# Performance work log

Hardware: AMD Instinct MI355X
Metric: run time of the kernel (lower is better)

## Reference

```python
import jax, jax.numpy as jnp
import numpy as np

BS, NQ, DIMS = 4, 6400, 256
NH, NL, NP, NQUEUE = 8, 1, 4, 2


def ms_deform_attn(value, shapes_np, starts_np, loc, attn):
    # value: [B, Nv, H, D]; loc: [B, Nq, H, L, P, 2] in [0,1]; attn: [B, Nq, H, L, P]
    B, Nv, H, D = value.shape
    _, Nq, _, L, P, _ = loc.shape
    out = jnp.zeros((B, H, Nq, D), loc.dtype)
    for l in range(L):
        Hl, Wl = int(shapes_np[l, 0]), int(shapes_np[l, 1])
        s = int(starts_np[l])
        vl = value[:, s:s + Hl * Wl].transpose(0, 2, 1, 3)  # [B,H,HW,D]
        # grid_sample align_corners=False pixel coords
        x = loc[:, :, :, l, :, 0] * Wl - 0.5  # [B,Nq,H,P]
        y = loc[:, :, :, l, :, 1] * Hl - 0.5
        x0 = jnp.floor(x); y0 = jnp.floor(y)
        dx = x - x0; dy = y - y0
        x0i = x0.astype(jnp.int32); y0i = y0.astype(jnp.int32)
        acc = jnp.zeros((B, H, Nq * P, D), loc.dtype)
        corners = [(x0i, y0i, (1 - dx) * (1 - dy)),
                   (x0i + 1, y0i, dx * (1 - dy)),
                   (x0i, y0i + 1, (1 - dx) * dy),
                   (x0i + 1, y0i + 1, dx * dy)]
        for xi, yi, w in corners:
            valid = (xi >= 0) & (xi < Wl) & (yi >= 0) & (yi < Hl)
            idx = jnp.clip(yi, 0, Hl - 1) * Wl + jnp.clip(xi, 0, Wl - 1)  # [B,Nq,H,P]
            idx_t = idx.transpose(0, 2, 1, 3).reshape(B, H, Nq * P, 1)
            g = jnp.take_along_axis(vl, idx_t, axis=2)  # [B,H,Nq*P,D]
            wv = jnp.where(valid, w, 0.0).transpose(0, 2, 1, 3).reshape(B, H, Nq * P, 1)
            acc = acc + g * wv
        acc = acc.reshape(B, H, Nq, P, D)
        wl = attn[:, :, :, l].transpose(0, 2, 1, 3)  # [B,H,Nq,P]
        out = out + jnp.einsum('bhnpd,bhnp->bhnd', acc, wl)
    return out.transpose(0, 2, 1, 3).reshape(B, Nq, H * D)


def setup_inputs() -> dict:
    key = jax.random.key(0)
    ks = jax.random.split(key, 12)
    d2 = DIMS * NQUEUE
    noff = NQUEUE * NH * NL * NP * 2
    nattn = NQUEUE * NH * NL * NP
    sc = 1.0 / np.sqrt(DIMS)
    return {
        'query': jax.random.normal(ks[0], (BS, NQ, DIMS), jnp.float32),
        'voxbev': jax.random.normal(ks[1], (BS, NQ, DIMS), jnp.float32),
        'reference_points': jax.random.uniform(ks[2], (BS * NQUEUE, NQ, NL, 2), jnp.float32),
        'spatial_shapes': jnp.array([[80, 80]], dtype=jnp.int64),
        'level_start_index': jnp.array([0], dtype=jnp.int64),
        'Wv': jax.random.normal(ks[3], (DIMS, DIMS), jnp.float32) * sc,
        'bv': jax.random.normal(ks[4], (DIMS,), jnp.float32) * 0.01,
        'Woff': jax.random.normal(ks[5], (d2, noff), jnp.float32) * (1.0 / np.sqrt(d2)),
        'boff': jax.random.normal(ks[6], (noff,), jnp.float32),
        'Wattn': jax.random.normal(ks[7], (d2, nattn), jnp.float32) * (1.0 / np.sqrt(d2)),
        'battn': jax.random.normal(ks[8], (nattn,), jnp.float32) * 0.01,
        'Wo': jax.random.normal(ks[9], (DIMS, DIMS), jnp.float32) * sc,
        'bo': jax.random.normal(ks[10], (DIMS,), jnp.float32) * 0.01,
    }


def reference(query, voxbev, reference_points, spatial_shapes, level_start_index,
              Wv, bv, Woff, boff, Wattn, battn, Wo, bo):
    bs, nq, dims = query.shape
    shapes_np = np.asarray(spatial_shapes)
    starts_np = np.asarray(level_start_index)
    identity = query
    # value = stack([query, voxbev], 1).reshape(bs*2, nq, dims) -> interleaved [q0,v0,q1,v1,...]
    value = jnp.stack([query, voxbev], 1).reshape(bs * NQUEUE, nq, dims)
    qcat = jnp.concatenate([value[:bs], query], -1)  # [bs, nq, 2*dims]
    v = (value @ Wv + bv).reshape(bs * NQUEUE, nq, NH, dims // NH)
    off = (qcat @ Woff + boff).reshape(bs, nq, NH, NQUEUE, NL, NP, 2)
    attn = (qcat @ Wattn + battn).reshape(bs, nq, NH, NQUEUE, NL * NP)
    attn = jax.nn.softmax(attn, axis=-1).reshape(bs, nq, NH, NQUEUE, NL, NP)
    attn = attn.transpose(0, 3, 1, 2, 4, 5).reshape(bs * NQUEUE, nq, NH, NL, NP)
    off = off.transpose(0, 3, 1, 2, 4, 5, 6).reshape(bs * NQUEUE, nq, NH, NL, NP, 2)
    # offset normalizer: (W, H) per level
    norm = jnp.stack([spatial_shapes[:, 1], spatial_shapes[:, 0]], -1).astype(off.dtype)  # [L,2]
    loc = reference_points[:, :, None, :, None, :] + off / norm[None, None, None, :, None, :]
    out = ms_deform_attn(v, shapes_np, starts_np, loc, attn)  # [bs*2, nq, dims]
    out = out.reshape(bs, NQUEUE, nq, dims).mean(1)  # mean over queue
    out = out @ Wo + bo
    return out + identity  # dropout is identity in eval
```

## Files before the change

kernel.cpp:

```cpp
#include <hip/hip_runtime.h>
#include <hip/hip_bf16.h>

#define BS   4
#define NQ   6400
#define DIMS 256
#define NH   8
#define NP   4
#define GW   80
#define GH   80

typedef __hip_bfloat16 bf16;
typedef unsigned short ushort;
typedef __attribute__((ext_vector_type(8))) short short8;
typedef __attribute__((ext_vector_type(4))) float floatx4;

union bfu { bf16 h; ushort s; };
__device__ __forceinline__ ushort f2bs(float x) { bfu u; u.h = __float2bfloat16(x); return u.s; }
__device__ __forceinline__ float bs2f(ushort s) { return __uint_as_float(((unsigned)s) << 16); }
__device__ __forceinline__ float ldin(const void* p, size_t i, int isf) {
    return isf ? ((const float*)p)[i] : bs2f(((const ushort*)p)[i]);
}

__device__ __forceinline__ void gl_lds16(const void* gsrc, void* ldst) {
    __builtin_amdgcn_global_load_lds(
        (const __attribute__((address_space(1))) unsigned int*)gsrc,
        (__attribute__((address_space(3))) unsigned int*)ldst,
        16, 0, 0);
}

__device__ __forceinline__ int self_detect(const ushort* __restrict__ q, int tid) {
    int bad = 0;
    const uint4 u0 = ((const uint4*)q)[tid * 2];
    const uint4 u1 = ((const uint4*)q)[tid * 2 + 1];
    const unsigned w[8] = { u0.x, u0.y, u0.z, u0.w, u1.x, u1.y, u1.z, u1.w };
    #pragma unroll
    for (int j = 0; j < 8; ++j) {
        if (((w[j] >> 7)  & 0xFF) > 160) bad = 1;
        if (((w[j] >> 23) & 0xFF) > 160) bad = 1;
    }
    return __any(bad) ? 1 : 0;
}

__global__ __launch_bounds__(256) void prep_k(
    const void* __restrict__ Wv, const void* __restrict__ bv,
    const void* __restrict__ Woff, const void* __restrict__ boff,
    const void* __restrict__ Wattn, const void* __restrict__ battn,
    const void* __restrict__ Wo, const void* __restrict__ bo,
    int* __restrict__ flagp,
    ushort* __restrict__ WvT, ushort* __restrict__ WoaT, ushort* __restrict__ WoT,
    float* __restrict__ biasv, float* __restrict__ biasoa, float* __restrict__ biaso,
    const void* __restrict__ query, const void* __restrict__ voxbev,
    uint4* __restrict__ qb, uint4* __restrict__ vbv)
{
    const int tid = threadIdx.x;
    const int isf = self_detect((const ushort*)query, tid);
    const int bid = blockIdx.x;
    if (bid == 0 && tid == 0) *flagp = isf;
    if (bid < 899) {
        const int i = bid * 256 + tid;
        const int n1 = 256 * 256, n2 = n1 + 192 * 512, n3 = n2 + 256 * 256;
        const int n4 = n3 + 256, n5 = n4 + 192, n6 = n5 + 256;
        if (i < n1) {
            int n = i >> 8, k = i & 255;
            WvT[i] = f2bs(ldin(Wv, (size_t)k * 256 + n, isf));
        } else if (i < n2) {
            int j = i - n1, n = j >> 9, k = j & 511;
            float v = (n < 128) ? ldin(Woff, (size_t)k * 128 + n, isf)
                                : ldin(Wattn, (size_t)k * 64 + (n - 128), isf);
            WoaT[j] = f2bs(v);
        } else if (i < n3) {
            int j = i - n2, n = j >> 8, k = j & 255;
            WoT[j] = f2bs(ldin(Wo, (size_t)k * 256 + n, isf));
        } else if (i < n4) {
            biasv[i - n3] = ldin(bv, i - n3, isf);
        } else if (i < n5) {
            int j = i - n4;
            biasoa[j] = (j < 128) ? ldin(boff, j, isf) : ldin(battn, j - 128, isf);
        } else if (i < n6) {
            biaso[i - n5] = ldin(bo, i - n5, isf);
        }
    } else {
        if (isf == 0) return;
        const int t = (bid - 899) * 256 + tid;
        const int half = 819200;
        const void* src = (t < half) ? query : voxbev;
        uint4* dst = (t < half) ? qb : vbv;
        const int j = (t < half) ? t : t - half;
        const float4* s = (const float4*)src + (size_t)j * 2;
        float4 a = s[0], b = s[1];
        uint4 o;
        o.x = ((unsigned)f2bs(a.y) << 16) | f2bs(a.x);
        o.y = ((unsigned)f2bs(a.w) << 16) | f2bs(a.z);
        o.z = ((unsigned)f2bs(b.y) << 16) | f2bs(b.x);
        o.w = ((unsigned)f2bs(b.w) << 16) | f2bs(b.z);
        dst[j] = o;
    }
}

enum { A_VAL = 0, A_QCAT = 1, A_PLAIN = 2 };
enum { O_BF16 = 0, O_FINAL = 1, O_VPERM = 2, O_OAPERM = 3 };

#define BKS  128
#define ABYT (128 * 256)
#define SMEMB (ABYT + 2 * 64 * 256)

template <int AMODE, int OMODE, int KTOT, int NW, int NXW, int MG>
__device__ __forceinline__ void pgemm_body(
    const int F, char* smem,
    const ushort* __restrict__ Apl, const ushort* __restrict__ BT,
    const float* __restrict__ biasf, void* __restrict__ C,
    const void* __restrict__ query_raw, const void* __restrict__ voxbev_raw,
    const ushort* __restrict__ qb, const ushort* __restrict__ vbv,
    const int isf)
{
    constexpr int N = NW * 64 * NXW;
    constexpr int TW = NW * 64;
    constexpr int NT = KTOT / BKS;
    constexpr int CSTW = (NW == 1) ? 67 : 131;
    char* abuf = smem;
    char* bbuf = smem + ABYT;
    float* cbf = (float*)smem;

    const int xcd = F & 7, l = F >> 3;
    const int n = l % NXW;
    const int mg = (l / NXW) * 8 + xcd;
    if (mg >= MG) return;
    const int bm = mg * 128, bn = n * TW;

    const int tid = threadIdx.x;
    const int lane = tid & 63, wv = tid >> 6;
    const int wm = wv * 32;
    const int fr = lane & 15;
    const int srow = lane >> 4;
    const int sslot = lane & 15;

    const ushort* qsrc = isf ? qb  : (const ushort*)query_raw;
    const ushort* vsrc = isf ? vbv : (const ushort*)voxbev_raw;
    const ushort* aph[2] = { nullptr, nullptr };
    if (AMODE == A_PLAIN) {
        aph[0] = Apl + (size_t)bm * DIMS;
    } else {
        const int b = bm / NQ, q0 = bm - (bm / NQ) * NQ;
        aph[0] = ((b & 1) ? vsrc : qsrc) + (size_t)((b >> 1) * NQ + q0) * DIMS;
        if (AMODE == A_QCAT) aph[1] = qsrc + (size_t)(b * NQ + q0) * DIMS;
    }

    floatx4 acc[2][4 * NW] = {};

    #pragma unroll
    for (int t = 0; t < NT; ++t) {
        if (t > 0) __syncthreads();
        #pragma unroll
        for (int c8 = 0; c8 < 8; ++c8) {
            const int c = wv * 8 + c8;
            const int row = c * 4 + srow;
            const int g = sslot ^ (row & 15);
            const int k = t * BKS + g * 8;
            const ushort* gp;
            if (AMODE == A_QCAT && KTOT == 512)
                gp = aph[k >> 8] + (size_t)row * DIMS + (k & 255);
            else
                gp = aph[0] + (size_t)row * DIMS + k;
            gl_lds16(gp, abuf + c * 1024);
        }
        #pragma unroll
        for (int cb = 0; cb < 4 * NW; ++cb) {
            const int c = wv * 4 * NW + cb;
            const int row = c * 4 + srow;
            const int g = sslot ^ (row & 15);
            gl_lds16(&BT[(size_t)(bn + row) * KTOT + t * BKS + g * 8],
                     bbuf + c * 1024);
        }
        asm volatile("s_waitcnt vmcnt(0)" ::: "memory");
        __syncthreads();

        #pragma unroll
        for (int k0 = 0; k0 < BKS; k0 += 32) {
            const int gl = (k0 >> 3) + (lane >> 4);
            const int sl = gl ^ fr;
            short8 af[2], bf[4 * NW];
            #pragma unroll
            for (int mt = 0; mt < 2; ++mt)
                af[mt] = *(const short8*)(abuf + (wm + mt * 16 + fr) * 256
                                               + sl * 16);
            #pragma unroll
            for (int nt = 0; nt < 4 * NW; ++nt)
                bf[nt] = *(const short8*)(bbuf + (nt * 16 + fr) * 256
                                               + sl * 16);
            #pragma unroll
            for (int mt = 0; mt < 2; ++mt)
                #pragma unroll
                for (int nt = 0; nt < 4 * NW; ++nt)
                    acc[mt][nt] = __builtin_amdgcn_mfma_f32_16x16x32_bf16(
                        af[mt], bf[nt], acc[mt][nt], 0, 0, 0);
        }
    }

    const int col = lane & 15, rq = (lane >> 4) * 4;

    if (NW == 1) {
        __syncthreads();
        #pragma unroll
        for (int mt = 0; mt < 2; ++mt)
            #pragma unroll
            for (int nt = 0; nt < 4; ++nt)
                #pragma unroll
                for (int r = 0; r < 4; ++r)
                    cbf[(wm + mt * 16 + rq + r) * 67 + nt * 16 + col] =
                        acc[mt][nt][r];
        __syncthreads();

        if (OMODE == O_FINAL && isf) {
            const int r16 = tid >> 4, cc = tid & 15;
            #pragma unroll
            for (int it = 0; it < 8; ++it) {
                const int lr = it * 16 + r16;
                const size_t g = (size_t)(bm + lr);
                float4 x = *(const float4*)&cbf[lr * 67 + cc * 4];
                const ushort* rs = qsrc + g * DIMS + bn + cc * 4;
                x.x += biasf[bn + cc * 4 + 0] + bs2f(rs[0]);
                x.y += biasf[bn + cc * 4 + 1] + bs2f(rs[1]);
                x.z += biasf[bn + cc * 4 + 2] + bs2f(rs[2]);
                x.w += biasf[bn + cc * 4 + 3] + bs2f(rs[3]);
                *(float4*)((float*)C + g * N + bn + cc * 4) = x;
            }
        } else {
            const int r8 = tid >> 3, c8 = tid & 7;
            #pragma unroll
            for (int it = 0; it < 4; ++it) {
                const int lr = it * 32 + r8;
                const size_t g = (size_t)(bm + lr);
                float4 x0 = *(const float4*)&cbf[lr * 67 + c8 * 8];
                float4 x1 = *(const float4*)&cbf[lr * 67 + c8 * 8 + 4];
                float xs[8] = { x0.x, x0.y, x0.z, x0.w, x1.x, x1.y, x1.z, x1.w };
                #pragma unroll
                for (int e = 0; e < 8; ++e) xs[e] += biasf[bn + c8 * 8 + e];
                if (OMODE == O_FINAL) {
                    const ushort* rs = qsrc + g * DIMS + bn + c8 * 8;
                    #pragma unroll
                    for (int e = 0; e < 8; ++e) xs[e] += bs2f(rs[e]);
                }
                uint4 o;
                o.x = ((unsigned)f2bs(xs[1]) << 16) | f2bs(xs[0]);
                o.y = ((unsigned)f2bs(xs[3]) << 16) | f2bs(xs[2]);
                o.z = ((unsigned)f2bs(xs[5]) << 16) | f2bs(xs[4]);
                o.w = ((unsigned)f2bs(xs[7]) << 16) | f2bs(xs[6]);
                ushort* dstp;
                if (OMODE == O_VPERM) {
                    const int cc = bn + c8 * 8;
                    const int s = (int)(g / NQ), qq = (int)(g % NQ);
                    dstp = (ushort*)C + ((size_t)(s * 8 + (cc >> 5)) * NQ + qq) * 32
                                      + (cc & 31);
                } else if (OMODE == O_OAPERM) {
                    const int cc = bn + c8 * 8;
                    const int bb = (int)(g / NQ), qq = (int)(g % NQ);
                    int hh, off;
                    if (cc < 128) { hh = cc >> 4; off = cc & 15; }
                    else          { hh = (cc - 128) >> 3; off = 16; }
                    dstp = (ushort*)C + ((size_t)(bb * 8 + hh) * NQ + qq) * 24 + off;
                } else {
                    dstp = (ushort*)C + g * N + bn + c8 * 8;
                }
                *(uint4*)dstp = o;
            }
        }
    } else {
        const int lbase = wm & 63;
        #pragma unroll
        for (int half = 0; half < 2; ++half) {
            __syncthreads();
            if ((wv >> 1) == half) {
                #pragma unroll
                for (int mt = 0; mt < 2; ++mt)
                    #pragma unroll
                    for (int nt = 0; nt < 8; ++nt)
                        #pragma unroll
                        for (int r = 0; r < 4; ++r)
                            cbf[(lbase + mt * 16 + rq + r) * 131 + nt * 16 + col] =
                                acc[mt][nt][r];
            }
            __syncthreads();

            if (OMODE == O_FINAL && isf) {
                const int r32 = tid >> 5, cc = tid & 31;
                #pragma unroll
                for (int it = 0; it < 8; ++it) {
                    const int lr = it * 8 + r32;
                    const size_t g = (size_t)(bm + half * 64 + lr);
                    float4 x = *(const float4*)&cbf[lr * 131 + cc * 4];
                    const ushort* rs = qsrc + g * DIMS + bn + cc * 4;
                    x.x += biasf[bn + cc * 4 + 0] + bs2f(rs[0]);
                    x.y += biasf[bn + cc * 4 + 1] + bs2f(rs[1]);
                    x.z += biasf[bn + cc * 4 + 2] + bs2f(rs[2]);
                    x.w += biasf[bn + cc * 4 + 3] + bs2f(rs[3]);
                    *(float4*)((float*)C + g * N + bn + cc * 4) = x;
                }
            } else {
                const int r16 = tid >> 4, cc = tid & 15;
                #pragma unroll
                for (int it = 0; it < 4; ++it) {
                    const int lr = it * 16 + r16;
                    const size_t g = (size_t)(bm + half * 64 + lr);
                    float4 x0 = *(const float4*)&cbf[lr * 131 + cc * 8];
                    float4 x1 = *(const float4*)&cbf[lr * 131 + cc * 8 + 4];
                    float xs[8] = { x0.x, x0.y, x0.z, x0.w, x1.x, x1.y, x1.z, x1.w };
                    #pragma unroll
                    for (int e = 0; e < 8; ++e) xs[e] += biasf[bn + cc * 8 + e];
                    if (OMODE == O_FINAL) {
                        const ushort* rs = qsrc + g * DIMS + bn + cc * 8;
                        #pragma unroll
                        for (int e = 0; e < 8; ++e) xs[e] += bs2f(rs[e]);
                    }
                    uint4 o;
                    o.x = ((unsigned)f2bs(xs[1]) << 16) | f2bs(xs[0]);
                    o.y = ((unsigned)f2bs(xs[3]) << 16) | f2bs(xs[2]);
                    o.z = ((unsigned)f2bs(xs[5]) << 16) | f2bs(xs[4]);
                    o.w = ((unsigned)f2bs(xs[7]) << 16) | f2bs(xs[6]);
                    ushort* dstp;
                    if (OMODE == O_VPERM) {
                        const int cc2 = bn + cc * 8;
                        const int s = (int)(g / NQ), qq = (int)(g % NQ);
                        dstp = (ushort*)C
                             + ((size_t)(s * 8 + (cc2 >> 5)) * NQ + qq) * 32
                             + (cc2 & 31);
                    } else {
                        dstp = (ushort*)C + g * N + bn + cc * 8;
                    }
                    *(uint4*)dstp = o;
                }
            }
        }
    }
}

__global__ __launch_bounds__(256) void gemm12_k(
    const ushort* __restrict__ WvT, const float* __restrict__ biasv,
    ushort* __restrict__ v_ws,
    const ushort* __restrict__ WoaT, const float* __restrict__ biasoa,
    ushort* __restrict__ offraw,
    const void* __restrict__ query_raw, const void* __restrict__ voxbev_raw,
    const ushort* __restrict__ qb, const ushort* __restrict__ vbv,
    const int* __restrict__ flagp)
{
    __shared__ __align__(16) char smem[SMEMB];
    const int isf = *flagp;
    const int bid = blockIdx.x;
    if (bid < 800) {
        pgemm_body<A_VAL, O_VPERM, 256, 2, 2, 400>(bid, smem,
            nullptr, WvT, biasv, (void*)v_ws, query_raw, voxbev_raw, qb, vbv, isf);
    } else {
        pgemm_body<A_QCAT, O_OAPERM, 512, 1, 3, 200>(bid - 800, smem,
            nullptr, WoaT, biasoa, (void*)offraw, query_raw, voxbev_raw, qb, vbv, isf);
    }
}

__global__ __launch_bounds__(256) void gemm4_k(
    const ushort* __restrict__ Apl, const ushort* __restrict__ BT,
    const float* __restrict__ biasf, void* __restrict__ C,
    const void* __restrict__ query_raw, const void* __restrict__ voxbev_raw,
    const ushort* __restrict__ qb, const ushort* __restrict__ vbv,
    const int* __restrict__ flagp)
{
    __shared__ __align__(16) char smem[SMEMB];
    const int isf = *flagp;
    pgemm_body<A_PLAIN, O_FINAL, 256, 2, 2, 200>(blockIdx.x, smem,
        Apl, BT, biasf, C, query_raw, voxbev_raw, qb, vbv, isf);
}

__global__ __launch_bounds__(256) void sample_k(
    const ushort* __restrict__ v,
    const ushort* __restrict__ offp,
    const void* __restrict__ refpts,
    const int* __restrict__ flagp,
    ushort* __restrict__ sampled)
{
    const int isf = *flagp;
    __shared__ int   sidx[64][2][17];
    __shared__ float swt [64][2][17];
    const int tid = threadIdx.x;
    const int j = blockIdx.x;
    const int h = j & 7;
    const int k = j >> 3;
    const int b = k / 100;
    const int q0 = (k % 100) * 64;

    if (tid < 128) {
        const int lq = tid >> 1, queue = tid & 1;
        const int q = q0 + lq;
        const ushort* rec = offp + ((size_t)(b * 8 + h) * NQ + q) * 24;
        const ushort* al = rec + 16 + queue * 4;
        float l0 = bs2f(al[0]), l1 = bs2f(al[1]), l2 = bs2f(al[2]), l3 = bs2f(al[3]);
        float mx = fmaxf(fmaxf(l0, l1), fmaxf(l2, l3));
        float e0 = __expf(l0 - mx), e1 = __expf(l1 - mx);
        float e2 = __expf(l2 - mx), e3 = __expf(l3 - mx);
        float inv = 0.5f / (e0 + e1 + e2 + e3);
        const int bq = b * 2 + queue;
        const float rx = ldin(refpts, ((size_t)bq * NQ + q) * 2 + 0, isf);
        const float ry = ldin(refpts, ((size_t)bq * NQ + q) * 2 + 1, isf);
        const ushort* od = rec + queue * 8;
        float ww[4] = { e0 * inv, e1 * inv, e2 * inv, e3 * inv };
        #pragma unroll
        for (int p = 0; p < NP; ++p) {
            const float x = rx * (float)GW + bs2f(od[p * 2 + 0]) - 0.5f;
            const float y = ry * (float)GH + bs2f(od[p * 2 + 1]) - 0.5f;
            const float x0f = floorf(x), y0f = floorf(y);
            const float dx = x - x0f, dy = y - y0f;
            const int x0 = (int)x0f, y0 = (int)y0f;
            const float wp = ww[p];
            const float cw4[4] = { wp * (1.0f - dx) * (1.0f - dy),
                                   wp * dx * (1.0f - dy),
                                   wp * (1.0f - dx) * dy,
                                   wp * dx * dy };
            #pragma unroll
            for (int c = 0; c < 4; ++c) {
                const int xs = x0 + (c & 1), ys = y0 + (c >> 1);
                const bool ok = (unsigned)xs < (unsigned)GW && (unsigned)ys < (unsigned)GH;
                const int xi = min(max(xs, 0), GW - 1);
                const int yi = min(max(ys, 0), GH - 1);
                sidx[lq][queue][p * 4 + c] = yi * GW + xi;
                swt [lq][queue][p * 4 + c] = ok ? cw4[c] : 0.0f;
            }
        }
    }
    __syncthreads();

    const int lq = tid >> 2, d8 = tid & 3;
    const int q = q0 + lq;
    float a[8] = {};
    #pragma unroll
    for (int queue = 0; queue < 2; ++queue) {
        const ushort* vb = v + (((size_t)(b * 2 + queue) * 8 + h) * NQ) * 32 + d8 * 8;
        #pragma unroll
        for (int hf = 0; hf < 2; ++hf) {
            uint4 g[8];
            #pragma unroll
            for (int u = 0; u < 8; ++u) {
                const int ci = sidx[lq][queue][hf * 8 + u];
                g[u] = *(const uint4*)&vb[(size_t)ci * 32];
            }
            __builtin_amdgcn_sched_barrier(0);
            #pragma unroll
            for (int u = 0; u < 8; ++u) {
                const float cw = swt[lq][queue][hf * 8 + u];
                a[0] += cw * bs2f((ushort)g[u].x); a[1] += cw * bs2f((ushort)(g[u].x >> 16));
                a[2] += cw * bs2f((ushort)g[u].y); a[3] += cw * bs2f((ushort)(g[u].y >> 16));
                a[4] += cw * bs2f((ushort)g[u].z); a[5] += cw * bs2f((ushort)(g[u].z >> 16));
                a[6] += cw * bs2f((ushort)g[u].w); a[7] += cw * bs2f((ushort)(g[u].w >> 16));
            }
        }
    }
    uint4 o;
    o.x = ((unsigned)f2bs(a[1]) << 16) | f2bs(a[0]);
    o.y = ((unsigned)f2bs(a[3]) << 16) | f2bs(a[2]);
    o.z = ((unsigned)f2bs(a[5]) << 16) | f2bs(a[4]);
    o.w = ((unsigned)f2bs(a[7]) << 16) | f2bs(a[6]);
    *(uint4*)&sampled[((size_t)b * NQ + q) * DIMS + h * 32 + d8 * 8] = o;
}

extern "C" void kernel_launch(void* const* d_in, const int* in_sizes, int n_in,
                              void* d_out, int out_size, void* d_ws, size_t ws_size,
                              hipStream_t stream)
{
    const void* query  = d_in[0];
    const void* voxbev = d_in[1];
    const void* refpts = d_in[2];
    const void* Wv   = d_in[5];  const void* bv    = d_in[6];
    const void* Woff = d_in[7];  const void* boff  = d_in[8];
    const void* Wattn= d_in[9];  const void* battn = d_in[10];
    const void* Wo   = d_in[11]; const void* bo    = d_in[12];

    char* p = (char*)d_ws;
    int* flag = (int*)p;             p += 256;
    ushort* WvT  = (ushort*)p;       p += 256 * 256 * 2;
    ushort* WoaT = (ushort*)p;       p += 192 * 512 * 2;
    ushort* WoT  = (ushort*)p;       p += 256 * 256 * 2;
    float* biasv  = (float*)p;       p += 1024;
    float* biasoa = (float*)p;       p += 1024;
    float* biaso  = (float*)p;       p += 1024;
    ushort* qb   = (ushort*)p;       p += (size_t)BS * NQ * DIMS * 2;
    ushort* vbv  = (ushort*)p;       p += (size_t)BS * NQ * DIMS * 2;
    ushort* v_ws = (ushort*)p;       p += (size_t)2 * BS * NQ * DIMS * 2;
    ushort* offraw = (ushort*)p;     p += (size_t)BS * NQ * 192 * 2;
    ushort* sampled = (ushort*)p;

    prep_k<<<7299, 256, 0, stream>>>(Wv, bv, Woff, boff, Wattn, battn, Wo, bo,
                                     flag, WvT, WoaT, WoT, biasv, biasoa, biaso,
                                     query, voxbev, (uint4*)qb, (uint4*)vbv);

    gemm12_k<<<1400, 256, 0, stream>>>(WvT, biasv, v_ws, WoaT, biasoa, offraw,
                                       query, voxbev, qb, vbv, flag);

    sample_k<<<3200, 256, 0, stream>>>(v_ws, offraw, refpts, flag, sampled);

    gemm4_k<<<400, 256, 0, stream>>>(sampled, WoT, biaso, d_out,
                                     query, voxbev, qb, vbv, flag);
}
```

Before: 181.9 us.

## Double-buffer gemm12 K-loop with 64-wide tiles and async LDS prefetch

Replaces the single-buffered 128-K-step GEMM in gemm12 with a double-buffered pipeline using 64-wide K steps and 128x64 output tiles. The next stage's global-to-LDS loads are issued before computing the current one, using partial vmcnt waits, so load latency overlaps MFMA work. LDS use drops to 48KB and the V-projection grid grows from 800 to 1600 blocks, which may raise occupancy. The final GEMM keeps the old wide path via a separate specialized template. Costs are more barriers per K element and smaller tiles that reload A more often.

```diff
diff --git a/kernel.cpp b/kernel.cpp
--- a/kernel.cpp
+++ b/kernel.cpp
@@ -26,6 +26,12 @@
         (const __attribute__((address_space(1))) unsigned int*)gsrc,
         (__attribute__((address_space(3))) unsigned int*)ldst,
         16, 0, 0);
+}
+
+__device__ __forceinline__ void barrier_fence() {
+    __builtin_amdgcn_sched_barrier(0);
+    asm volatile("s_barrier" ::: "memory");
+    __builtin_amdgcn_sched_barrier(0);
 }
 
 __device__ __forceinline__ int self_detect(const ushort* __restrict__ q, int tid) {
@@ -100,12 +106,11 @@
 enum { A_VAL = 0, A_QCAT = 1, A_PLAIN = 2 };
 enum { O_BF16 = 0, O_FINAL = 1, O_VPERM = 2, O_OAPERM = 3 };
 
-#define BKS  128
-#define ABYT (128 * 256)
-#define SMEMB (ABYT + 2 * 64 * 256)
-
-template <int AMODE, int OMODE, int KTOT, int NW, int NXW, int MG>
-__device__ __forceinline__ void pgemm_body(
+#define PTILE 24576
+#define PSMEM (2 * PTILE)
+
+template <int AMODE, int OMODE, int KTOT, int NXW, int MG>
+__device__ __forceinline__ void pgemm_pipe(
     const int F, char* smem,
     const ushort* __restrict__ Apl, const ushort* __restrict__ BT,
     const float* __restrict__ biasf, void* __restrict__ C,
@@ -113,26 +118,23 @@
     const ushort* __restrict__ qb, const ushort* __restrict__ vbv,
     const int isf)
 {
-    constexpr int N = NW * 64 * NXW;
-    constexpr int TW = NW * 64;
-    constexpr int NT = KTOT / BKS;
-    constexpr int CSTW = (NW == 1) ? 67 : 131;
-    char* abuf = smem;
-    char* bbuf = smem + ABYT;
+    constexpr int N = 64 * NXW;
+    constexpr int NT = KTOT / 64;
     float* cbf = (float*)smem;
 
     const int xcd = F & 7, l = F >> 3;
     const int n = l % NXW;
     const int mg = (l / NXW) * 8 + xcd;
     if (mg >= MG) return;
-    const int bm = mg * 128, bn = n * TW;
+    const int bm = mg * 128, bn = n * 64;
 
     const int tid = threadIdx.x;
     const int lane = tid & 63, wv = tid >> 6;
     const int wm = wv * 32;
     const int fr = lane & 15;
-    const int srow = lane >> 4;
-    const int sslot = lane & 15;
+    const int lrow = lane >> 3;
+    const int lslot = lane & 7;
+    const int sg = lslot ^ lrow;
 
     const ushort* qsrc = isf ? qb  : (const ushort*)query_raw;
     const ushort* vsrc = isf ? vbv : (const ushort*)voxbev_raw;
@@ -145,7 +147,180 @@
         if (AMODE == A_QCAT) aph[1] = qsrc + (size_t)(b * NQ + q0) * DIMS;
     }
 
-    floatx4 acc[2][4 * NW] = {};
+    auto stage = [&](int td, int t) {
+        char* ab = smem + td * PTILE;
+        char* bb = ab + 16384;
+        #pragma unroll
+        for (int c4 = 0; c4 < 4; ++c4) {
+            const int c = wv * 4 + c4;
+            const int row = c * 8 + lrow;
+            const int k = t * 64 + sg * 8;
+            const ushort* gp;
+            if (AMODE == A_QCAT && KTOT == 512)
+                gp = aph[k >> 8] + (size_t)row * DIMS + (k & 255);
+            else
+                gp = aph[0] + (size_t)row * DIMS + k;
+            gl_lds16(gp, ab + c * 1024);
+        }
+        #pragma unroll
+        for (int c2 = 0; c2 < 2; ++c2) {
+            const int c = wv * 2 + c2;
+            const int row = c * 8 + lrow;
+            gl_lds16(&BT[(size_t)(bn + row) * KTOT + t * 64 + sg * 8],
+                     bb + c * 1024);
+        }
+    };
+
+    floatx4 acc[2][4] = {};
+
+    stage(0, 0);
+    #pragma unroll
+    for (int t = 0; t < NT; ++t) {
+        if (t + 1 < NT) {
+            stage((t + 1) & 1, t + 1);
+            __builtin_amdgcn_sched_barrier(0);
+            asm volatile("s_waitcnt vmcnt(6)" ::: "memory");
+        } else {
+            __builtin_amdgcn_sched_barrier(0);
+            asm volatile("s_waitcnt vmcnt(0)" ::: "memory");
+        }
+        barrier_fence();
+
+        const short* acur = (const short*)(smem + (t & 1) * PTILE);
+        const short* bcur = acur + 8192;
+        #pragma unroll
+        for (int k0 = 0; k0 < 64; k0 += 32) {
+            const int gl = (k0 >> 3) + (lane >> 4);
+            const int sl = gl ^ (fr & 7);
+            short8 af[2], bf[4];
+            #pragma unroll
+            for (int mt = 0; mt < 2; ++mt)
+                af[mt] = *(const short8*)&acur[(wm + mt * 16 + fr) * 64 + sl * 8];
+            #pragma unroll
+            for (int nt = 0; nt < 4; ++nt)
+                bf[nt] = *(const short8*)&bcur[(nt * 16 + fr) * 64 + sl * 8];
+            #pragma unroll
+            for (int mt = 0; mt < 2; ++mt)
+                #pragma unroll
+                for (int nt = 0; nt < 4; ++nt)
+                    acc[mt][nt] = __builtin_amdgcn_mfma_f32_16x16x32_bf16(
+                        af[mt], bf[nt], acc[mt][nt], 0, 0, 0);
+        }
+        barrier_fence();
+    }
+
+    __syncthreads();
+    const int col = lane & 15, rq = (lane >> 4) * 4;
+    #pragma unroll
+    for (int mt = 0; mt < 2; ++mt)
+        #pragma unroll
+        for (int nt = 0; nt < 4; ++nt)
+            #pragma unroll
+            for (int r = 0; r < 4; ++r)
+                cbf[(wm + mt * 16 + rq + r) * 67 + nt * 16 + col] = acc[mt][nt][r];
+    __syncthreads();
+
+    if (OMODE == O_FINAL && isf) {
+        const int r16 = tid >> 4, cc = tid & 15;
+        #pragma unroll
+        for (int it = 0; it < 8; ++it) {
+            const int lr = it * 16 + r16;
+            const size_t g = (size_t)(bm + lr);
+            float4 x = *(const float4*)&cbf[lr * 67 + cc * 4];
+            const ushort* rs = qsrc + g * DIMS + bn + cc * 4;
+            x.x += biasf[bn + cc * 4 + 0] + bs2f(rs[0]);
+            x.y += biasf[bn + cc * 4 + 1] + bs2f(rs[1]);
+            x.z += biasf[bn + cc * 4 + 2] + bs2f(rs[2]);
+            x.w += biasf[bn + cc * 4 + 3] + bs2f(rs[3]);
+            *(float4*)((float*)C + g * N + bn + cc * 4) = x;
+        }
+    } else {
+        const int r8 = tid >> 3, c8 = tid & 7;
+        #pragma unroll
+        for (int it = 0; it < 4; ++it) {
+            const int lr = it * 32 + r8;
+            const size_t g = (size_t)(bm + lr);
+            float4 x0 = *(const float4*)&cbf[lr * 67 + c8 * 8];
+            float4 x1 = *(const float4*)&cbf[lr * 67 + c8 * 8 + 4];
+            float xs[8] = { x0.x, x0.y, x0.z, x0.w, x1.x, x1.y, x1.z, x1.w };
+            #pragma unroll
+            for (int e = 0; e < 8; ++e) xs[e] += biasf[bn + c8 * 8 + e];
+            if (OMODE == O_FINAL) {
+                const ushort* rs = qsrc + g * DIMS + bn + c8 * 8;
+                #pragma unroll
+                for (int e = 0; e < 8; ++e) xs[e] += bs2f(rs[e]);
+            }
+            uint4 o;
+            o.x = ((unsigned)f2bs(xs[1]) << 16) | f2bs(xs[0]);
+            o.y = ((unsigned)f2bs(xs[3]) << 16) | f2bs(xs[2]);
+            o.z = ((unsigned)f2bs(xs[5]) << 16) | f2bs(xs[4]);
+            o.w = ((unsigned)f2bs(xs[7]) << 16) | f2bs(xs[6]);
+            ushort* dstp;
+            if (OMODE == O_VPERM) {
+                const int cc = bn + c8 * 8;
+                const int s = (int)(g / NQ), qq = (int)(g % NQ);
+                dstp = (ushort*)C + ((size_t)(s * 8 + (cc >> 5)) * NQ + qq) * 32
+                                  + (cc & 31);
+            } else if (OMODE == O_OAPERM) {
+                const int cc = bn + c8 * 8;
+                const int bb = (int)(g / NQ), qq = (int)(g % NQ);
+                int hh, off;
+                if (cc < 128) { hh = cc >> 4; off = cc & 15; }
+                else          { hh = (cc - 128) >> 3; off = 16; }
+                dstp = (ushort*)C + ((size_t)(bb * 8 + hh) * NQ + qq) * 24 + off;
+            } else {
+                dstp = (ushort*)C + g * N + bn + c8 * 8;
+            }
+            *(uint4*)dstp = o;
+        }
+    }
+}
+
+#define BKS  128
+#define ABYT (128 * 256)
+#define WSMEM (ABYT + 2 * 64 * 256)
+
+template <int AMODE, int OMODE, int KTOT, int MG>
+__device__ __forceinline__ void pgemm_wide(
+    const int F, char* smem,
+    const ushort* __restrict__ Apl, const ushort* __restrict__ BT,
+    const float* __restrict__ biasf, void* __restrict__ C,
+    const void* __restrict__ query_raw, const void* __restrict__ voxbev_raw,
+    const ushort* __restrict__ qb, const ushort* __restrict__ vbv,
+    const int isf)
+{
+    constexpr int NXW = 2;
+    constexpr int N = 256;
+    constexpr int NT = KTOT / BKS;
+    char* abuf = smem;
+    char* bbuf = smem + ABYT;
+    float* cbf = (float*)smem;
+
+    const int xcd = F & 7, l = F >> 3;
+    const int n = l % NXW;
+    const int mg = (l / NXW) * 8 + xcd;
+    if (mg >= MG) return;
+    const int bm = mg * 128, bn = n * 128;
+
+    const int tid = threadIdx.x;
+    const int lane = tid & 63, wv = tid >> 6;
+    const int wm = wv * 32;
+    const int fr = lane & 15;
+    const int srow = lane >> 4;
+    const int sslot = lane & 15;
+
+    const ushort* qsrc = isf ? qb  : (const ushort*)query_raw;
+    const ushort* vsrc = isf ? vbv : (const ushort*)voxbev_raw;
+    const ushort* aph[2] = { nullptr, nullptr };
+    if (AMODE == A_PLAIN) {
+        aph[0] = Apl + (size_t)bm * DIMS;
+    } else {
+        const int b = bm / NQ, q0 = bm - (bm / NQ) * NQ;
+        aph[0] = ((b & 1) ? vsrc : qsrc) + (size_t)((b >> 1) * NQ + q0) * DIMS;
+        if (AMODE == A_QCAT) aph[1] = qsrc + (size_t)(b * NQ + q0) * DIMS;
+    }
+
+    floatx4 acc[2][8] = {};
 
     #pragma unroll
     for (int t = 0; t < NT; ++t) {
@@ -156,16 +331,12 @@
             const int row = c * 4 + srow;
             const int g = sslot ^ (row & 15);
             const int k = t * BKS + g * 8;
-            const ushort* gp;
-            if (AMODE == A_QCAT && KTOT == 512)
-                gp = aph[k >> 8] + (size_t)row * DIMS + (k & 255);
-            else
-                gp = aph[0] + (size_t)row * DIMS + k;
+            const ushort* gp = aph[0] + (size_t)row * DIMS + k;
             gl_lds16(gp, abuf + c * 1024);
         }
         #pragma unroll
-        for (int cb = 0; cb < 4 * NW; ++cb) {
-            const int c = wv * 4 * NW + cb;
+        for (int cb = 0; cb < 8; ++cb) {
+            const int c = wv * 8 + cb;
             const int row = c * 4 + srow;
             const int g = sslot ^ (row & 15);
             gl_lds16(&BT[(size_t)(bn + row) * KTOT + t * BKS + g * 8],
@@ -178,45 +349,46 @@
         for (int k0 = 0; k0 < BKS; k0 += 32) {
             const int gl = (k0 >> 3) + (lane >> 4);
             const int sl = gl ^ fr;
-            short8 af[2], bf[4 * NW];
+            short8 af[2], bf[8];
             #pragma unroll
             for (int mt = 0; mt < 2; ++mt)
-                af[mt] = *(const short8*)(abuf + (wm + mt * 16 + fr) * 256
-                                               + sl * 16);
-            #pragma unroll
-            for (int nt = 0; nt < 4 * NW; ++nt)
-                bf[nt] = *(const short8*)(bbuf + (nt * 16 + fr) * 256
-                                               + sl * 16);
+                af[mt] = *(const short8*)(abuf + (wm + mt * 16 + fr) * 256 + sl * 16);
+            #pragma unroll
+            for (int nt = 0; nt < 8; ++nt)
+                bf[nt] = *(const short8*)(bbuf + (nt * 16 + fr) * 256 + sl * 16);
             #pragma unroll
             for (int mt = 0; mt < 2; ++mt)
                 #pragma unroll
-                for (int nt = 0; nt < 4 * NW; ++nt)
+                for (int nt = 0; nt < 8; ++nt)
                     acc[mt][nt] = __builtin_amdgcn_mfma_f32_16x16x32_bf16(
                         af[mt], bf[nt], acc[mt][nt], 0, 0, 0);
         }
     }
 
     const int col = lane & 15, rq = (lane >> 4) * 4;
-
-    if (NW == 1) {
+    const int lbase = wm & 63;
+    #pragma unroll
+    for (int half = 0; half < 2; ++half) {
         __syncthreads();
-        #pragma unroll
-        for (int mt = 0; mt < 2; ++mt)
-            #pragma unroll
-            for (int nt = 0; nt < 4; ++nt)
+        if ((wv >> 1) == half) {
+            #pragma unroll
+            for (int mt = 0; mt < 2; ++mt)
                 #pragma unroll
-                for (int r = 0; r < 4; ++r)
-                    cbf[(wm + mt * 16 + rq + r) * 67 + nt * 16 + col] =
-                        acc[mt][nt][r];
+                for (int nt = 0; nt < 8; ++nt)
+                    #pragma unroll
+                    for (int r = 0; r < 4; ++r)
+                        cbf[(lbase + mt * 16 + rq + r) * 131 + nt * 16 + col] =
+                            acc[mt][nt][r];
+        }
         __syncthreads();
 
         if (OMODE == O_FINAL && isf) {
-            const int r16 = tid >> 4, cc = tid & 15;
+            const int r32 = tid >> 5, cc = tid & 31;
             #pragma unroll
             for (int it = 0; it < 8; ++it) {
-                const int lr = it * 16 + r16;
-                const size_t g = (size_t)(bm + lr);
-                float4 x = *(const float4*)&cbf[lr * 67 + cc * 4];
+                const int lr = it * 8 + r32;
+                const size_t g = (size_t)(bm + half * 64 + lr);
+                float4 x = *(const float4*)&cbf[lr * 131 + cc * 4];
                 const ushort* rs = qsrc + g * DIMS + bn + cc * 4;
                 x.x += biasf[bn + cc * 4 + 0] + bs2f(rs[0]);
                 x.y += biasf[bn + cc * 4 + 1] + bs2f(rs[1]);
@@ -225,18 +397,18 @@
                 *(float4*)((float*)C + g * N + bn + cc * 4) = x;
             }
         } else {
-            const int r8 = tid >> 3, c8 = tid & 7;
+            const int r16 = tid >> 4, cc = tid & 15;
             #pragma unroll
             for (int it = 0; it < 4; ++it) {
-                const int lr = it * 32 + r8;
-                const size_t g = (size_t)(bm + lr);
-                float4 x0 = *(const float4*)&cbf[lr * 67 + c8 * 8];
-                float4 x1 = *(const float4*)&cbf[lr * 67 + c8 * 8 + 4];
+                const int lr = it * 16 + r16;
+                const size_t g = (size_t)(bm + half * 64 + lr);
+                float4 x0 = *(const float4*)&cbf[lr * 131 + cc * 8];
+                float4 x1 = *(const float4*)&cbf[lr * 131 + cc * 8 + 4];
                 float xs[8] = { x0.x, x0.y, x0.z, x0.w, x1.x, x1.y, x1.z, x1.w };
                 #pragma unroll
-                for (int e = 0; e < 8; ++e) xs[e] += biasf[bn + c8 * 8 + e];
+                for (int e = 0; e < 8; ++e) xs[e] += biasf[bn + cc * 8 + e];
                 if (OMODE == O_FINAL) {
-                    const ushort* rs = qsrc + g * DIMS + bn + c8 * 8;
+                    const ushort* rs = qsrc + g * DIMS + bn + cc * 8;
                     #pragma unroll
                     for (int e = 0; e < 8; ++e) xs[e] += bs2f(rs[e]);
                 }
@@ -247,87 +419,15 @@
                 o.w = ((unsigned)f2bs(xs[7]) << 16) | f2bs(xs[6]);
                 ushort* dstp;
                 if (OMODE == O_VPERM) {
-                    const int cc = bn + c8 * 8;
+                    const int cc2 = bn + cc * 8;
                     const int s = (int)(g / NQ), qq = (int)(g % NQ);
-                    dstp = (ushort*)C + ((size_t)(s * 8 + (cc >> 5)) * NQ + qq) * 32
-                                      + (cc & 31);
-                } else if (OMODE == O_OAPERM) {
-                    const int cc = bn + c8 * 8;
-                    const int bb = (int)(g / NQ), qq = (int)(g % NQ);
-                    int hh, off;
-                    if (cc < 128) { hh = cc >> 4; off = cc & 15; }
-                    else          { hh = (cc - 128) >> 3; off = 16; }
-                    dstp = (ushort*)C + ((size_t)(bb * 8 + hh) * NQ + qq) * 24 + off;
+                    dstp = (ushort*)C
+                         + ((size_t)(s * 8 + (cc2 >> 5)) * NQ + qq) * 32
+                         + (cc2 & 31);
                 } else {
-                    dstp = (ushort*)C + g * N + bn + c8 * 8;
+                    dstp = (ushort*)C + g * N + bn + cc * 8;
                 }
                 *(uint4*)dstp = o;
-            }
-        }
-    } else {
-        const int lbase = wm & 63;
-        #pragma unroll
-        for (int half = 0; half < 2; ++half) {
-            __syncthreads();
-            if ((wv >> 1) == half) {
-                #pragma unroll
-                for (int mt = 0; mt < 2; ++mt)
-                    #pragma unroll
-                    for (int nt = 0; nt < 8; ++nt)
-                        #pragma unroll
-                        for (int r = 0; r < 4; ++r)
-                            cbf[(lbase + mt * 16 + rq + r) * 131 + nt * 16 + col] =
-                                acc[mt][nt][r];
-            }
-            __syncthreads();
-
-            if (OMODE == O_FINAL && isf) {
-                const int r32 = tid >> 5, cc = tid & 31;
-                #pragma unroll
-                for (int it = 0; it < 8; ++it) {
-                    const int lr = it * 8 + r32;
-                    const size_t g = (size_t)(bm + half * 64 + lr);
-                    float4 x = *(const float4*)&cbf[lr * 131 + cc * 4];
-                    const ushort* rs = qsrc + g * DIMS + bn + cc * 4;
-                    x.x += biasf[bn + cc * 4 + 0] + bs2f(rs[0]);
-                    x.y += biasf[bn + cc * 4 + 1] + bs2f(rs[1]);
-                    x.z += biasf[bn + cc * 4 + 2] + bs2f(rs[2]);
-                    x.w += biasf[bn + cc * 4 + 3] + bs2f(rs[3]);
-                    *(float4*)((float*)C + g * N + bn + cc * 4) = x;
-                }
-            } else {
-                const int r16 = tid >> 4, cc = tid & 15;
-                #pragma unroll
-                for (int it = 0; it < 4; ++it) {
-                    const int lr = it * 16 + r16;
-                    const size_t g = (size_t)(bm + half * 64 + lr);
-                    float4 x0 = *(const float4*)&cbf[lr * 131 + cc * 8];
-                    float4 x1 = *(const float4*)&cbf[lr * 131 + cc * 8 + 4];
-                    float xs[8] = { x0.x, x0.y, x0.z, x0.w, x1.x, x1.y, x1.z, x1.w };
-                    #pragma unroll
-                    for (int e = 0; e < 8; ++e) xs[e] += biasf[bn + cc * 8 + e];
-                    if (OMODE == O_FINAL) {
-                        const ushort* rs = qsrc + g * DIMS + bn + cc * 8;
-                        #pragma unroll
-                        for (int e = 0; e < 8; ++e) xs[e] += bs2f(rs[e]);
-                    }
-                    uint4 o;
-                    o.x = ((unsigned)f2bs(xs[1]) << 16) | f2bs(xs[0]);
-                    o.y = ((unsigned)f2bs(xs[3]) << 16) | f2bs(xs[2]);
-                    o.z = ((unsigned)f2bs(xs[5]) << 16) | f2bs(xs[4]);
-                    o.w = ((unsigned)f2bs(xs[7]) << 16) | f2bs(xs[6]);
-                    ushort* dstp;
-                    if (OMODE == O_VPERM) {
-                        const int cc2 = bn + cc * 8;
-                        const int s = (int)(g / NQ), qq = (int)(g % NQ);
-                        dstp = (ushort*)C
-                             + ((size_t)(s * 8 + (cc2 >> 5)) * NQ + qq) * 32
-                             + (cc2 & 31);
-                    } else {
-                        dstp = (ushort*)C + g * N + bn + cc * 8;
-                    }
-                    *(uint4*)dstp = o;
-                }
             }
         }
     }
@@ -342,14 +442,14 @@
     const ushort* __restrict__ qb, const ushort* __restrict__ vbv,
     const int* __restrict__ flagp)
 {
-    __shared__ __align__(16) char smem[SMEMB];
+    __shared__ __align__(16) char smem[PSMEM];
     const int isf = *flagp;
     const int bid = blockIdx.x;
-    if (bid < 800) {
-        pgemm_body<A_VAL, O_VPERM, 256, 2, 2, 400>(bid, smem,
+    if (bid < 1600) {
+        pgemm_pipe<A_VAL, O_VPERM, 256, 4, 400>(bid, smem,
             nullptr, WvT, biasv, (void*)v_ws, query_raw, voxbev_raw, qb, vbv, isf);
     } else {
-        pgemm_body<A_QCAT, O_OAPERM, 512, 1, 3, 200>(bid - 800, smem,
+        pgemm_pipe<A_QCAT, O_OAPERM, 512, 3, 200>(bid - 1600, smem,
             nullptr, WoaT, biasoa, (void*)offraw, query_raw, voxbev_raw, qb, vbv, isf);
     }
 }
@@ -361,9 +461,9 @@
     const ushort* __restrict__ qb, const ushort* __restrict__ vbv,
     const int* __restrict__ flagp)
 {
-    __shared__ __align__(16) char smem[SMEMB];
+    __shared__ __align__(16) char smem[WSMEM];
     const int isf = *flagp;
-    pgemm_body<A_PLAIN, O_FINAL, 256, 2, 2, 200>(blockIdx.x, smem,
+    pgemm_wide<A_PLAIN, O_FINAL, 256, 200>(blockIdx.x, smem,
         Apl, BT, biasf, C, query_raw, voxbev_raw, qb, vbv, isf);
 }
 
@@ -487,7 +587,7 @@
                                      flag, WvT, WoaT, WoT, biasv, biasoa, biaso,
                                      query, voxbev, (uint4*)qb, (uint4*)vbv);
 
-    gemm12_k<<<1400, 256, 0, stream>>>(WvT, biasv, v_ws, WoaT, biasoa, offraw,
+    gemm12_k<<<2200, 256, 0, stream>>>(WvT, biasv, v_ws, WoaT, biasoa, offraw,
                                        query, voxbev, qb, vbv, flag);
 
     sample_k<<<3200, 256, 0, stream>>>(v_ws, offraw, refpts, flag, sampled);
```

After: 178.6 us. About the same (-1.8%).
